# Kernel optimization log

Hardware: AMD Instinct MI355X
Metric: run time of the kernel (lower is better)

The kernel has to match this reference:

```python
import jax, jax.numpy as jnp
import numpy as np
from jax import lax

B, T, C, F_IN = 16, 128, 64, 128
H, FO = 4, 16          # GAT heads, out-features per head (gat_out)
HID = 32               # LSTM hidden (bidirectional -> 64)
NCLS = 3
TOPK, THR, TEMP = 2, 0.3, 1.5


def _layernorm(x, g, b, eps=1e-5):
    m = x.mean(-1, keepdims=True)
    v = ((x - m) ** 2).mean(-1, keepdims=True)
    return (x - m) / jnp.sqrt(v + eps) * g + b


def setup_inputs() -> dict:
    key = jax.random.key(0)
    ks = jax.random.split(key, 16)
    def lin(k, o, i):
        return jax.random.normal(k, (o, i), jnp.float32) / np.sqrt(i)
    return {
        "x": jax.random.uniform(ks[0], (B, T, C, F_IN), jnp.float32),
        "spec_w": jnp.ones((C, F_IN), jnp.float32),
        "gat_W": lin(ks[1], H * FO, F_IN),
        "gat_a": jax.random.normal(ks[2], (H, 2 * FO), jnp.float32),
        "gat_norm_g": jnp.ones((H * FO,), jnp.float32),
        "gat_norm_b": jnp.zeros((H * FO,), jnp.float32),
        "gat_res_W": lin(ks[3], H * FO, F_IN),
        "gat_res_b": jnp.zeros((H * FO,), jnp.float32),
        "lW_ih_f": lin(ks[4], 4 * HID, H * FO),
        "lW_hh_f": lin(ks[5], 4 * HID, HID),
        "lb_ih_f": jnp.zeros((4 * HID,), jnp.float32),
        "lb_hh_f": jnp.zeros((4 * HID,), jnp.float32),
        "lW_ih_b": lin(ks[6], 4 * HID, H * FO),
        "lW_hh_b": lin(ks[7], 4 * HID, HID),
        "lb_ih_b": jnp.zeros((4 * HID,), jnp.float32),
        "lb_hh_b": jnp.zeros((4 * HID,), jnp.float32),
        "ta_W": lin(ks[8], 2 * HID, 2 * HID),
        "ta_b": jnp.zeros((2 * HID,), jnp.float32),
        "ta_v": lin(ks[9], 1, 2 * HID),
        "cp_W": lin(ks[10], 1, 2 * HID),
        "cp_b": jnp.zeros((1,), jnp.float32),
        "norm_g": jnp.ones((2 * HID,), jnp.float32),
        "norm_b": jnp.zeros((2 * HID,), jnp.float32),
        "fc1_W": lin(ks[11], 32, 2 * HID),
        "fc1_b": jnp.zeros((32,), jnp.float32),
        "fc2_W": lin(ks[12], NCLS, 32),
        "fc2_b": jnp.zeros((NCLS,), jnp.float32),
    }


def _lstm(xs, Wih, Whh, bih, bhh):
    # xs: [T, N, in] -> [T, N, HID]; PyTorch gate order i,f,g,o
    N = xs.shape[1]
    def step(carry, xt):
        h, c = carry
        z = xt @ Wih.T + h @ Whh.T + bih + bhh
        i, f, g, o = jnp.split(z, 4, axis=-1)
        c = jax.nn.sigmoid(f) * c + jax.nn.sigmoid(i) * jnp.tanh(g)
        h = jax.nn.sigmoid(o) * jnp.tanh(c)
        return (h, c), h
    init = (jnp.zeros((N, HID), xs.dtype), jnp.zeros((N, HID), xs.dtype))
    return lax.scan(step, init, xs)[1]


def reference(x, spec_w, gat_W, gat_a, gat_norm_g, gat_norm_b, gat_res_W, gat_res_b,
              lW_ih_f, lW_hh_f, lb_ih_f, lb_hh_f, lW_ih_b, lW_hh_b, lb_ih_b, lb_hh_b,
              ta_W, ta_b, ta_v, cp_W, cp_b, norm_g, norm_b,
              fc1_W, fc1_b, fc2_W, fc2_b):
    # --- spectral weighting ---
    x = x * jax.nn.sigmoid(spec_w)                               # [B,T,C,F]
    # --- per-sample correlation graph (vectorized over B,T) ---
    Hn = x / (jnp.linalg.norm(x, axis=-1, keepdims=True) + 1e-8)
    A = jnp.einsum('btcf,btdf->bcd', Hn, Hn) / T                 # mean over T
    A = 0.5 * (A + jnp.swapaxes(A, 1, 2))
    # --- sparsify: per-row top-(k+1), threshold, off-diagonal, symmetrize ---
    _, idx = lax.top_k(A, TOPK + 1)                              # [B,C,k+1]
    topm = jax.nn.one_hot(idx, C).sum(axis=2) > 0                # [B,C,C]
    eye = jnp.eye(C, dtype=bool)
    keep = topm & (A > THR) & ~eye
    keep = keep | jnp.swapaxes(keep, 1, 2)
    A_s = jnp.where(keep, A, 0.0)                                # [B,C,C]
    # --- multi-head GAT, vectorized over all timesteps ---
    Wh = jnp.einsum('btcf,gf->btcg', x, gat_W).reshape(B, T, C, H, FO)
    ei = jnp.einsum('btchf,hf->btch', Wh, gat_a[:, :FO])
    ej = jnp.einsum('btchf,hf->btch', Wh, gat_a[:, FO:])
    e = ei[:, :, :, None, :] + ej[:, :, None, :, :]              # [B,T,C,C,H]
    e = jnp.where(e > 0, e, 0.2 * e)                             # LeakyReLU(0.2)
    mask = (A_s > 0) | eye                                       # [B,C,C]
    e = jnp.where(mask[:, None, :, :, None], e, -1e9)
    An = A_s / (A_s.sum(-1, keepdims=True) + 1e-8)
    e = e + An[:, None, :, :, None]
    alpha = jax.nn.softmax(e / TEMP, axis=3)                     # over j
    Hout = jnp.einsum('btijh,btjhf->btihf', alpha, Wh).reshape(B, T, C, H * FO)
    res = jnp.einsum('btcf,gf->btcg', x, gat_res_W) + gat_res_b
    g = jax.nn.relu(_layernorm(Hout + res, gat_norm_g, gat_norm_b))  # [B,T,C,64]
    # --- BiLSTM over T for each (faithful torch .view on [B,T,C,Fp]) ---
    seq = g.reshape(B * C, T, H * FO)
    xs = jnp.swapaxes(seq, 0, 1)                                 # [T,N,64]
    hf = _lstm(xs, lW_ih_f, lW_hh_f, lb_ih_f, lb_hh_f)
    hb = _lstm(xs[::-1], lW_ih_b, lW_hh_b, lb_ih_b, lb_hh_b)[::-1]
    h = jnp.swapaxes(jnp.concatenate([hf, hb], -1), 0, 1)        # [N,T,64]
    # --- temporal attention ---
    sc = (jnp.tanh(h @ ta_W.T + ta_b) @ ta_v.T)[..., 0]          # [N,T]
    al = jax.nn.softmax(sc / TEMP, axis=1)
    hp = (h * al[..., None]).sum(1)                              # [N,64]
    # --- channel attention pooling ---
    xc = hp.reshape(B, C, 2 * HID)
    w = jax.nn.softmax(xc @ cp_W.T + cp_b, axis=1)               # [B,C,1]
    pooled = (xc * w).sum(1)                                     # [B,64]
    pooled = _layernorm(pooled, norm_g, norm_b)
    hid = jax.nn.relu(pooled @ fc1_W.T + fc1_b)
    return hid @ fc2_W.T + fc2_b                                 # [B,3]
```

## Files before the change

kernel.cpp:

```cpp
#include <hip/hip_runtime.h>
#include <math.h>

#define BB 16
#define TT 128
#define CC 64
#define FF 128

static constexpr float INV_TEMP = 1.0f / 1.5f;

static constexpr size_t OFF_WTT   = 8192;
static constexpr size_t OFF_RTT   = 16384;
static constexpr size_t OFF_TAWT  = 24576;
static constexpr size_t OFF_AN    = 28672;
static constexpr size_t OFF_A     = 94208;
static constexpr size_t OFF_G     = 1208320;
static constexpr size_t OFF_H     = 9596928;
static constexpr size_t OFF_HP    = 17985536;
static constexpr size_t OFF_WIHT  = 18051072;
static constexpr size_t OFF_ZX    = 18067456;
static constexpr size_t OFF_WHS   = OFF_ZX + 16777216;
static constexpr size_t OFF_RS    = OFF_ZX + 25165824;
static constexpr size_t OFF_APART = OFF_WHS;

__global__ __launch_bounds__(256) void k_prep(const float* __restrict__ gat_W,
                                              const float* __restrict__ gat_rW,
                                              const float* __restrict__ ta_W,
                                              const float* __restrict__ Wihf,
                                              const float* __restrict__ Wihb,
                                              float* __restrict__ ws) {
    int i = blockIdx.x * 256 + threadIdx.x;
    if (i < 8192) {
        int k = i >> 6, g = i & 63;
        ws[OFF_WTT + i] = gat_W[g * 128 + k];
    } else if (i < 16384) {
        int j = i - 8192; int k = j >> 6, g = j & 63;
        ws[OFF_RTT + j] = gat_rW[g * 128 + k];
    } else if (i < 20480) {
        int j = i - 16384; int v = j >> 6, u = j & 63;
        ws[OFF_TAWT + j] = ta_W[u * 64 + v];
    } else if (i < 36864) {
        int j = i - 20480;
        int dir = j >> 13, rem = j & 8191, k = rem >> 7, gg = rem & 127;
        const float* W = dir ? Wihb : Wihf;
        ws[OFF_WIHT + j] = W[gg * 64 + k];
    }
}

__device__ __forceinline__ float4 sigmul4(const float4 xv, const float4 wv) {
    float4 o;
    o.x = xv.x / (1.f + __expf(-wv.x));
    o.y = xv.y / (1.f + __expf(-wv.y));
    o.z = xv.z / (1.f + __expf(-wv.z));
    o.w = xv.w / (1.f + __expf(-wv.w));
    return o;
}

__global__ __launch_bounds__(256) void k_corr(const float* __restrict__ x,
                                              const float* __restrict__ spec_w,
                                              float* __restrict__ ws) {
    __shared__ __align__(16) float tile[64 * 132];
    __shared__ float rn[64];
    const int ch = blockIdx.x, b = blockIdx.y, tid = threadIdx.x;
    const int lane = tid & 63, wave = tid >> 6;
    const int c0 = wave * 16 + ((lane >> 4) << 2);
    const int d0 = (lane & 15) << 2;
    const float4* __restrict__ sg4 = (const float4*)spec_w;
    float acc[4][4];
#pragma unroll
    for (int a = 0; a < 4; ++a)
#pragma unroll
        for (int e = 0; e < 4; ++e) acc[a][e] = 0.f;

    for (int t8 = 0; t8 < 2; ++t8) {
        const int t = ch * 2 + t8;
        __syncthreads();
        const float4* __restrict__ xp4 = (const float4*)(x + ((size_t)(b * TT + t)) * CC * FF);
        for (int i4 = tid; i4 < 2048; i4 += 256) {
            const int row = i4 >> 5, col4 = i4 & 31;
            *(float4*)&tile[row * 132 + col4 * 4] = sigmul4(xp4[i4], sg4[i4]);
        }
        __syncthreads();
        {
            const int row = tid >> 2, part = tid & 3;
            const float4* tr = (const float4*)(tile + row * 132 + part * 32);
            float s = 0.f;
#pragma unroll
            for (int q = 0; q < 8; ++q) {
                const float4 v = tr[q];
                s += v.x * v.x + v.y * v.y + v.z * v.z + v.w * v.w;
            }
            s += __shfl_xor(s, 1); s += __shfl_xor(s, 2);
            if (part == 0) rn[row] = 1.f / (sqrtf(s) + 1e-8f);
        }
        __syncthreads();
        float dot[4][4];
#pragma unroll
        for (int a = 0; a < 4; ++a)
#pragma unroll
            for (int e = 0; e < 4; ++e) dot[a][e] = 0.f;
        for (int f4 = 0; f4 < 32; ++f4) {
            float4 xc4[4], xd4[4];
#pragma unroll
            for (int a = 0; a < 4; ++a) xc4[a] = *(const float4*)&tile[(c0 + a) * 132 + f4 * 4];
#pragma unroll
            for (int e = 0; e < 4; ++e) xd4[e] = *(const float4*)&tile[(d0 + e) * 132 + f4 * 4];
#pragma unroll
            for (int a = 0; a < 4; ++a)
#pragma unroll
                for (int e = 0; e < 4; ++e)
                    dot[a][e] += xc4[a].x * xd4[e].x + xc4[a].y * xd4[e].y +
                                 xc4[a].z * xd4[e].z + xc4[a].w * xd4[e].w;
        }
#pragma unroll
        for (int a = 0; a < 4; ++a) {
            const float ra = rn[c0 + a];
#pragma unroll
            for (int e = 0; e < 4; ++e) acc[a][e] += ra * rn[d0 + e] * dot[a][e];
        }
    }
    float* __restrict__ Ap = ws + OFF_APART + ((size_t)(b * 64 + ch)) * 4096;
#pragma unroll
    for (int a = 0; a < 4; ++a)
#pragma unroll
        for (int e = 0; e < 4; ++e) Ap[(c0 + a) * 64 + d0 + e] = acc[a][e];
}

__global__ __launch_bounds__(256) void k_reduceA(float* __restrict__ ws) {
    int i = blockIdx.x * 256 + threadIdx.x;
    int b = i >> 12, e = i & 4095;
    const float* Ap = ws + OFF_APART + (size_t)b * 64 * 4096;
    float s = 0.f;
#pragma unroll 8
    for (int ch = 0; ch < 64; ++ch) s += Ap[ch * 4096 + e];
    ws[OFF_A + i] = s * (1.f / 128.f);
}

__global__ __launch_bounds__(64) void k_sparsify(float* __restrict__ ws) {
    __shared__ float As[64 * 65];
    __shared__ unsigned char kp[64 * 64];
    const int b = blockIdx.x, tid = threadIdx.x;
    const float* Ag = ws + OFF_A + (size_t)b * 4096;
    for (int m = 0; m < 64; ++m) As[m * 65 + tid] = Ag[m * 64 + tid];
    __syncthreads();
    const int c = tid;
    int s0 = -1, s1 = -1, s2 = -1;
    for (int p = 0; p < 3; ++p) {
        float best = -1e30f; int bi = -1;
        for (int d = 0; d < 64; ++d) {
            if (d == s0 || d == s1) continue;
            float v = As[c * 65 + d];
            if (v > best) { best = v; bi = d; }
        }
        if (p == 0) s0 = bi; else if (p == 1) s1 = bi; else s2 = bi;
    }
    for (int d = 0; d < 64; ++d) {
        float v = As[c * 65 + d];
        kp[c * 64 + d] = (unsigned char)(((d == s0) | (d == s1) | (d == s2)) &&
                                         (v > 0.3f) && (d != c));
    }
    __syncthreads();
    float rs = 0.f;
    for (int d = 0; d < 64; ++d) {
        bool k2 = kp[c * 64 + d] || kp[d * 64 + c];
        rs += k2 ? As[c * 65 + d] : 0.f;
    }
    const float inv = 1.f / (rs + 1e-8f);
    float* An = ws + OFF_AN + (size_t)b * 4096;
    for (int d = 0; d < 64; ++d) {
        bool k2 = kp[c * 64 + d] || kp[d * 64 + c];
        An[c * 64 + d] = k2 ? As[c * 65 + d] * inv : 0.f;
    }
}

__global__ __launch_bounds__(256) void k_wh(const float* __restrict__ x,
                                            const float* __restrict__ spec_w,
                                            const float* __restrict__ wt,
                                            const float* __restrict__ rt,
                                            float* __restrict__ whs,
                                            float* __restrict__ rs,
                                            const float* __restrict__ res_b) {
    __shared__ __align__(16) float tile[64 * 132];
    const int bt = blockIdx.x, tid = threadIdx.x;
    const float4* __restrict__ xp4 = (const float4*)(x + (size_t)bt * 8192);
    const float4* __restrict__ sg4 = (const float4*)spec_w;
    for (int i4 = tid; i4 < 2048; i4 += 256) {
        const int row = i4 >> 5, col4 = i4 & 31;
        *(float4*)&tile[row * 132 + col4 * 4] = sigmul4(xp4[i4], sg4[i4]);
    }
    __syncthreads();
    const int tx = tid & 31, ty = tid >> 5;
    const int mat = tx >> 4, cx = tx & 15;
    const int r0 = ty * 8, c0 = cx * 4;
    const float* __restrict__ wbase = mat ? rt : wt;
    float acc[8][4];
#pragma unroll
    for (int i = 0; i < 8; ++i)
#pragma unroll
        for (int j = 0; j < 4; ++j) acc[i][j] = 0.f;
    for (int k4 = 0; k4 < 32; ++k4) {
        float xs[8][4];
#pragma unroll
        for (int i = 0; i < 8; ++i) {
            const float4 v = *(const float4*)&tile[(r0 + i) * 132 + k4 * 4];
            xs[i][0] = v.x; xs[i][1] = v.y; xs[i][2] = v.z; xs[i][3] = v.w;
        }
#pragma unroll
        for (int kk = 0; kk < 4; ++kk) {
            const float4 wv = *(const float4*)(wbase + (k4 * 4 + kk) * 64 + c0);
#pragma unroll
            for (int i = 0; i < 8; ++i) {
                acc[i][0] += xs[i][kk] * wv.x;
                acc[i][1] += xs[i][kk] * wv.y;
                acc[i][2] += xs[i][kk] * wv.z;
                acc[i][3] += xs[i][kk] * wv.w;
            }
        }
    }
    if (mat == 0) {
        float* __restrict__ op = whs + (size_t)bt * 4096;
#pragma unroll
        for (int i = 0; i < 8; ++i) {
            float4 o; o.x = acc[i][0]; o.y = acc[i][1]; o.z = acc[i][2]; o.w = acc[i][3];
            *(float4*)(op + (r0 + i) * 64 + c0) = o;
        }
    } else {
        const float4 rb = *(const float4*)(res_b + c0);
        float* __restrict__ op = rs + (size_t)bt * 4096;
#pragma unroll
        for (int i = 0; i < 8; ++i) {
            float4 o; o.x = acc[i][0] + rb.x; o.y = acc[i][1] + rb.y;
            o.z = acc[i][2] + rb.z; o.w = acc[i][3] + rb.w;
            *(float4*)(op + (r0 + i) * 64 + c0) = o;
        }
    }
}

__global__ __launch_bounds__(256) void k_att(const float* __restrict__ ws,
                                             const float* __restrict__ whs,
                                             const float* __restrict__ rs,
                                             float* __restrict__ g,
                                             const float* __restrict__ gat_a,
                                             const float* __restrict__ ln_g,
                                             const float* __restrict__ ln_b) {
    __shared__ __align__(16) float sWh[64 * 68];
    __shared__ float sAn[64 * 65];
    __shared__ float sEjT[256];
    __shared__ float sStat[64 * 8];
    const int t = blockIdx.x, b = blockIdx.y, tid = threadIdx.x;
    const size_t bt = (size_t)(b * TT + t);
    const float4* __restrict__ wh4 = (const float4*)(whs + bt * 4096);
    for (int i4 = tid; i4 < 1024; i4 += 256) {
        const int row = i4 >> 4, c4 = i4 & 15;
        *(float4*)&sWh[row * 68 + c4 * 4] = wh4[i4];
    }
    const float* __restrict__ ang = ws + OFF_AN + (size_t)b * 4096;
    for (int i = tid; i < 4096; i += 256) sAn[(i >> 6) * 65 + (i & 63)] = ang[i];
    __syncthreads();

    const int ia = tid & 63, ha = tid >> 6;
    float eiv = 0.f, ejv = 0.f;
    {
        const float* __restrict__ whrow = sWh + ia * 68 + ha * 16;
        const float* __restrict__ aip = gat_a + ha * 32;
#pragma unroll
        for (int q = 0; q < 16; ++q) {
            const float w = whrow[q];
            eiv += w * aip[q];
            ejv += w * aip[16 + q];
        }
    }
    sEjT[ha * 64 + ia] = ejv;
    __syncthreads();

    float ao[16];
#pragma unroll
    for (int f = 0; f < 16; ++f) ao[f] = 0.f;
    float sum = 0.f;
    const float* __restrict__ anrow = sAn + ia * 65;
    const float* __restrict__ ejrow = sEjT + ha * 64;
#pragma unroll 4
    for (int j = 0; j < 64; ++j) {
        const float s = eiv + ejrow[j];
        const float l = s > 0.f ? s : 0.2f * s;
        const float anv = anrow[j];
        const float z = (anv != 0.f || j == ia) ? (l + anv) : -1e9f;
        const float p = __expf(z * INV_TEMP);
        sum += p;
        const float* __restrict__ wj = sWh + j * 68 + ha * 16;
        const float4 w0 = *(const float4*)(wj);
        const float4 w1 = *(const float4*)(wj + 4);
        const float4 w2 = *(const float4*)(wj + 8);
        const float4 w3 = *(const float4*)(wj + 12);
        ao[0]  += p * w0.x; ao[1]  += p * w0.y; ao[2]  += p * w0.z; ao[3]  += p * w0.w;
        ao[4]  += p * w1.x; ao[5]  += p * w1.y; ao[6]  += p * w1.z; ao[7]  += p * w1.w;
        ao[8]  += p * w2.x; ao[9]  += p * w2.y; ao[10] += p * w2.z; ao[11] += p * w2.w;
        ao[12] += p * w3.x; ao[13] += p * w3.y; ao[14] += p * w3.z; ao[15] += p * w3.w;
    }
    const float inv = 1.f / sum;
    float val[16];
    float s1 = 0.f, s2 = 0.f;
    const float* __restrict__ rsp = rs + bt * 4096 + ia * 64 + ha * 16;
#pragma unroll
    for (int q = 0; q < 4; ++q) {
        const float4 rv = *(const float4*)(rsp + q * 4);
        val[q * 4 + 0] = ao[q * 4 + 0] * inv + rv.x;
        val[q * 4 + 1] = ao[q * 4 + 1] * inv + rv.y;
        val[q * 4 + 2] = ao[q * 4 + 2] * inv + rv.z;
        val[q * 4 + 3] = ao[q * 4 + 3] * inv + rv.w;
    }
#pragma unroll
    for (int f = 0; f < 16; ++f) { s1 += val[f]; s2 += val[f] * val[f]; }
    sStat[ia * 8 + ha] = s1;
    sStat[ia * 8 + 4 + ha] = s2;
    __syncthreads();
    const float tsum = sStat[ia * 8 + 0] + sStat[ia * 8 + 1] + sStat[ia * 8 + 2] + sStat[ia * 8 + 3];
    const float tsq  = sStat[ia * 8 + 4] + sStat[ia * 8 + 5] + sStat[ia * 8 + 6] + sStat[ia * 8 + 7];
    const float mean = tsum * (1.f / 64.f);
    const float var = tsq * (1.f / 64.f) - mean * mean;
    const float rstd = rsqrtf(var + 1e-5f);
    float* __restrict__ gout = g + bt * 4096 + ia * 64 + ha * 16;
#pragma unroll
    for (int q = 0; q < 4; ++q) {
        const float4 gm = *(const float4*)(ln_g + ha * 16 + q * 4);
        const float4 bt4 = *(const float4*)(ln_b + ha * 16 + q * 4);
        float4 o;
        o.x = fmaxf((val[q * 4 + 0] - mean) * rstd * gm.x + bt4.x, 0.f);
        o.y = fmaxf((val[q * 4 + 1] - mean) * rstd * gm.y + bt4.y, 0.f);
        o.z = fmaxf((val[q * 4 + 2] - mean) * rstd * gm.z + bt4.z, 0.f);
        o.w = fmaxf((val[q * 4 + 3] - mean) * rstd * gm.w + bt4.w, 0.f);
        *(float4*)(gout + q * 4) = o;
    }
}

__global__ __launch_bounds__(256) void k_zx(const float* __restrict__ gbuf,
                                            const float* __restrict__ ws,
                                            float* __restrict__ zx,
                                            const float* __restrict__ bihf, const float* __restrict__ bhhf,
                                            const float* __restrict__ bihb, const float* __restrict__ bhhb) {
    __shared__ __align__(16) float gS[128 * 68];
    const int mt2 = blockIdx.x, dir = blockIdx.y, tid = threadIdx.x;
    const float4* __restrict__ gsrc4 = (const float4*)(gbuf + (size_t)mt2 * 8192);
    for (int i4 = tid; i4 < 2048; i4 += 256) {
        const int row = i4 >> 4, c4 = i4 & 15;
        *(float4*)&gS[row * 68 + c4 * 4] = gsrc4[i4];
    }
    __syncthreads();
    const int ty = tid >> 4, cxx = tid & 15;
    const int c0 = cxx * 8;
    const float* __restrict__ wT = ws + OFF_WIHT + (size_t)dir * 8192;
    float acc[8][8];
#pragma unroll
    for (int i = 0; i < 8; ++i)
#pragma unroll
        for (int j = 0; j < 8; ++j) acc[i][j] = 0.f;
    for (int k4 = 0; k4 < 16; ++k4) {
        float xs[8][4];
#pragma unroll
        for (int i = 0; i < 8; ++i) {
            const float4 v = *(const float4*)&gS[(ty + 16 * i) * 68 + k4 * 4];
            xs[i][0] = v.x; xs[i][1] = v.y; xs[i][2] = v.z; xs[i][3] = v.w;
        }
#pragma unroll
        for (int kk = 0; kk < 4; ++kk) {
            const float4 w0 = *(const float4*)(wT + (k4 * 4 + kk) * 128 + c0);
            const float4 w1 = *(const float4*)(wT + (k4 * 4 + kk) * 128 + c0 + 4);
#pragma unroll
            for (int i = 0; i < 8; ++i) {
                const float xv = xs[i][kk];
                acc[i][0] += xv * w0.x; acc[i][1] += xv * w0.y;
                acc[i][2] += xv * w0.z; acc[i][3] += xv * w0.w;
                acc[i][4] += xv * w1.x; acc[i][5] += xv * w1.y;
                acc[i][6] += xv * w1.z; acc[i][7] += xv * w1.w;
            }
        }
    }
    const float* bi = dir ? bihb : bihf;
    const float* bh = dir ? bhhb : bhhf;
    float bsum[8];
    {
        const float4 b0 = *(const float4*)(bi + c0), b1 = *(const float4*)(bi + c0 + 4);
        const float4 h0 = *(const float4*)(bh + c0), h1 = *(const float4*)(bh + c0 + 4);
        bsum[0] = b0.x + h0.x; bsum[1] = b0.y + h0.y; bsum[2] = b0.z + h0.z; bsum[3] = b0.w + h0.w;
        bsum[4] = b1.x + h1.x; bsum[5] = b1.y + h1.y; bsum[6] = b1.z + h1.z; bsum[7] = b1.w + h1.w;
    }
    float* __restrict__ zrow = zx + (size_t)dir * 16777216 + (size_t)mt2 * 16384;
#pragma unroll
    for (int i = 0; i < 8; ++i) {
        const int r = ty + 16 * i;
        float4 o0, o1;
        o0.x = acc[i][0] + bsum[0]; o0.y = acc[i][1] + bsum[1];
        o0.z = acc[i][2] + bsum[2]; o0.w = acc[i][3] + bsum[3];
        o1.x = acc[i][4] + bsum[4]; o1.y = acc[i][5] + bsum[5];
        o1.z = acc[i][6] + bsum[6]; o1.w = acc[i][7] + bsum[7];
        *(float4*)&zrow[r * 128 + c0] = o0;
        *(float4*)&zrow[r * 128 + c0 + 4] = o1;
    }
}

__device__ __forceinline__ float rl(float v, int l) {
    return __int_as_float(__builtin_amdgcn_readlane(__float_as_int(v), l));
}

__global__ __launch_bounds__(64, 1) void k_lstm6(const float* __restrict__ zx,
                                                 float* __restrict__ hbuf,
                                                 const float* __restrict__ Whhf,
                                                 const float* __restrict__ Whhb) {
    __shared__ __align__(16) float swb[128 * 36];
    const int n = blockIdx.x, dir = blockIdx.y, r = threadIdx.x;
    const bool lo = (r < 32);
    const float* __restrict__ Whh = dir ? Whhb : Whhf;
    const float4* W4 = (const float4*)Whh;
    {
        float4* sw = (float4*)swb;
#pragma unroll
        for (int m = 0; m < 16; ++m) {
            const int idx = r + 64 * m;
            const int j = idx >> 3, q = idx & 7;
            sw[j * 9 + q] = W4[idx];
        }
    }
    __syncthreads();
    const float4* sw4 = (const float4*)swb;
    int baseA = r * 9;
    int baseB = (r + 64) * 9;
    const float* __restrict__ zxp = zx + (size_t)dir * 16777216 + (size_t)n * 16384;
    float* __restrict__ hout = hbuf + (size_t)n * 8192 + dir * 32 + r;
    float hv = 0.f, cv = 0.f;

#define SADDR(S_) (zxp + (size_t)(dir ? 127 - (S_) : (S_)) * 128)
#define DOTQL(Q) {                                                          \
        const float4 u = sw4[baseA + Q];                                    \
        const float4 v = sw4[baseB + Q];                                    \
        const float h0 = rl(hv, 4 * Q + 0), h1 = rl(hv, 4 * Q + 1);         \
        const float h2 = rl(hv, 4 * Q + 2), h3 = rl(hv, 4 * Q + 3);         \
        a0 += h0 * u.x; b0 += h0 * v.x;                                     \
        a1 += h1 * u.y; b1 += h1 * v.y;                                     \
        a0 += h2 * u.z; b0 += h2 * v.z;                                     \
        a1 += h3 * u.w; b1 += h3 * v.w;                                     \
    }
#define STEP(S_, ZA, ZB) {                                                  \
        asm volatile("" : "+v"(baseA), "+v"(baseB));                        \
        float a0 = (ZA), a1 = 0.f, b0 = (ZB), b1 = 0.f;                     \
        DOTQL(0) DOTQL(1) DOTQL(2) DOTQL(3)                                 \
        DOTQL(4) DOTQL(5) DOTQL(6) DOTQL(7)                                 \
        const float zi = a0 + a1, zg = b0 + b1;                             \
        const float eA = __expf(-zi);                                       \
        const float sA = 1.f / (1.f + eA);                                  \
        const float eB = __expf(lo ? -2.f * zg : -zg);                      \
        const float vB = lo ? (2.f / (1.f + eB) - 1.f) : (1.f / (1.f + eB));\
        const float fv = __shfl_xor(sA, 32);                                \
        const float ox = __shfl_xor(vB, 32);                                \
        cv = fv * cv + sA * vB;                                             \
        const float eC = __expf(-2.f * cv);                                 \
        const float tc = 2.f / (1.f + eC) - 1.f;                            \
        hv = ox * tc;                                                       \
        const int s__ = dir ? 127 - (S_) : (S_);                            \
        if (lo) hout[s__ * 64] = hv;                                        \
    }

    const float* p0 = SADDR(0);
    const float* p1 = SADDR(1);
    float zA0 = p0[r], zB0 = p0[r + 64];
    float zA1 = p1[r], zB1 = p1[r + 64];
    for (int s2 = 0; s2 < 64; ++s2) {
        int sp = 2 * s2 + 2; if (sp > 126) sp = 126;
        const float* pn0 = SADDR(sp);
        const float* pn1 = SADDR(sp + 1);
        const float nA0 = pn0[r], nB0 = pn0[r + 64];
        const float nA1 = pn1[r], nB1 = pn1[r + 64];
        STEP(2 * s2, zA0, zB0);
        STEP(2 * s2 + 1, zA1, zB1);
        zA0 = nA0; zB0 = nB0; zA1 = nA1; zB1 = nB1;
    }
#undef STEP
#undef DOTQL
#undef SADDR
}

__global__ __launch_bounds__(256) void k_ta(float* __restrict__ ws,
                                            const float* __restrict__ tab,
                                            const float* __restrict__ tav) {
    __shared__ __align__(16) float hL[128 * 68];
    __shared__ float scL[128];
    __shared__ float sRed[4];
    __shared__ float sPart[256];
    const int n = blockIdx.x, tid = threadIdx.x, lane = tid & 63, wave = tid >> 6;
    const float4* __restrict__ hsrc4 = (const float4*)(ws + OFF_H + (size_t)n * 8192);
    for (int i4 = tid; i4 < 2048; i4 += 256) {
        const int row = i4 >> 4, c4 = i4 & 15;
        *(float4*)&hL[row * 68 + c4 * 4] = hsrc4[i4];
    }
    __syncthreads();
    const int ty8 = lane >> 3, ux = lane & 7;
    const int t0 = wave * 32 + ty8, u0 = ux * 8;
    const float* __restrict__ twt = ws + OFF_TAWT;
    float tb[8], tv[8];
    *(float4*)&tb[0] = *(const float4*)(tab + u0);
    *(float4*)&tb[4] = *(const float4*)(tab + u0 + 4);
    *(float4*)&tv[0] = *(const float4*)(tav + u0);
    *(float4*)&tv[4] = *(const float4*)(tav + u0 + 4);
    float a[4][8];
#pragma unroll
    for (int i = 0; i < 4; ++i)
#pragma unroll
        for (int j = 0; j < 8; ++j) a[i][j] = 0.f;
    for (int v4 = 0; v4 < 16; ++v4) {
        float xs[4][4];
#pragma unroll
        for (int i = 0; i < 4; ++i) {
            const float4 v = *(const float4*)&hL[(t0 + 8 * i) * 68 + v4 * 4];
            xs[i][0] = v.x; xs[i][1] = v.y; xs[i][2] = v.z; xs[i][3] = v.w;
        }
#pragma unroll
        for (int kk = 0; kk < 4; ++kk) {
            const float4 w0 = *(const float4*)(twt + (v4 * 4 + kk) * 64 + u0);
            const float4 w1 = *(const float4*)(twt + (v4 * 4 + kk) * 64 + u0 + 4);
#pragma unroll
            for (int i = 0; i < 4; ++i) {
                const float xv = xs[i][kk];
                a[i][0] += xv * w0.x; a[i][1] += xv * w0.y;
                a[i][2] += xv * w0.z; a[i][3] += xv * w0.w;
                a[i][4] += xv * w1.x; a[i][5] += xv * w1.y;
                a[i][6] += xv * w1.z; a[i][7] += xv * w1.w;
            }
        }
    }
#pragma unroll
    for (int i = 0; i < 4; ++i) {
        float s = 0.f;
#pragma unroll
        for (int u = 0; u < 8; ++u) s += tanhf(a[i][u] + tb[u]) * tv[u];
        s += __shfl_xor(s, 1); s += __shfl_xor(s, 2); s += __shfl_xor(s, 4);
        if (ux == 0) scL[t0 + 8 * i] = s;
    }
    __syncthreads();
    const float v = (tid < 128) ? scL[tid] : -1e30f;
    float mw = v;
    mw = fmaxf(mw, __shfl_xor(mw, 1)); mw = fmaxf(mw, __shfl_xor(mw, 2));
    mw = fmaxf(mw, __shfl_xor(mw, 4)); mw = fmaxf(mw, __shfl_xor(mw, 8));
    mw = fmaxf(mw, __shfl_xor(mw, 16)); mw = fmaxf(mw, __shfl_xor(mw, 32));
    if (lane == 0) sRed[wave] = mw;
    __syncthreads();
    const float m = fmaxf(fmaxf(sRed[0], sRed[1]), fmaxf(sRed[2], sRed[3]));
    const float p = (tid < 128) ? __expf((v - m) * INV_TEMP) : 0.f;
    float sw = p;
    sw += __shfl_xor(sw, 1); sw += __shfl_xor(sw, 2); sw += __shfl_xor(sw, 4);
    sw += __shfl_xor(sw, 8); sw += __shfl_xor(sw, 16); sw += __shfl_xor(sw, 32);
    __syncthreads();
    if (lane == 0) sRed[wave] = sw;
    __syncthreads();
    const float stot = sRed[0] + sRed[1] + sRed[2] + sRed[3];
    if (tid < 128) scL[tid] = p / stot;
    __syncthreads();
    float part = 0.f;
    for (int tt = 0; tt < 32; ++tt) {
        const int t = wave * 32 + tt;
        part += scL[t] * hL[t * 68 + lane];
    }
    sPart[wave * 64 + lane] = part;
    __syncthreads();
    if (tid < 64)
        ws[OFF_HP + (size_t)n * 64 + tid] =
            sPart[tid] + sPart[64 + tid] + sPart[128 + tid] + sPart[192 + tid];
}

__global__ __launch_bounds__(64) void k_final(const float* __restrict__ ws,
                                              const float* __restrict__ cpW, const float* __restrict__ cpb,
                                              const float* __restrict__ ng, const float* __restrict__ nb,
                                              const float* __restrict__ f1W, const float* __restrict__ f1b,
                                              const float* __restrict__ f2W, const float* __restrict__ f2b,
                                              float* __restrict__ out) {
    __shared__ float xc[64 * 65];
    __shared__ float wL[64];
    __shared__ float plL[64];
    __shared__ float h1L[32];
    const int b = blockIdx.x, tid = threadIdx.x;
    const float* hp = ws + OFF_HP + (size_t)b * 4096;
    for (int m = 0; m < 64; ++m) xc[m * 65 + tid] = hp[m * 64 + tid];
    __syncthreads();
    float s = cpb[0];
    for (int j = 0; j < 64; ++j) s += xc[tid * 65 + j] * cpW[j];
    float mm = s;
    for (int o = 1; o < 64; o <<= 1) mm = fmaxf(mm, __shfl_xor(mm, o));
    const float p = __expf(s - mm);
    float sum = p;
    for (int o = 1; o < 64; o <<= 1) sum += __shfl_xor(sum, o);
    wL[tid] = p / sum;
    __syncthreads();
    float pool = 0.f;
    for (int c = 0; c < 64; ++c) pool += xc[c * 65 + tid] * wL[c];
    float ms = pool;
    for (int o = 1; o < 64; o <<= 1) ms += __shfl_xor(ms, o);
    const float mean = ms * (1.f / 64.f);
    const float d = pool - mean;
    float vv = d * d;
    for (int o = 1; o < 64; o <<= 1) vv += __shfl_xor(vv, o);
    const float pl = d * rsqrtf(vv * (1.f / 64.f) + 1e-5f) * ng[tid] + nb[tid];
    plL[tid] = pl;
    __syncthreads();
    if (tid < 32) {
        float h1 = f1b[tid];
        for (int j = 0; j < 64; ++j) h1 += plL[j] * f1W[tid * 64 + j];
        h1L[tid] = fmaxf(h1, 0.f);
    }
    __syncthreads();
    if (tid < 3) {
        float o = f2b[tid];
        for (int uu = 0; uu < 32; ++uu) o += h1L[uu] * f2W[tid * 32 + uu];
        out[b * 3 + tid] = o;
    }
}

extern "C" void kernel_launch(void* const* d_in, const int* in_sizes, int n_in,
                              void* d_out, int out_size, void* d_ws, size_t ws_size,
                              hipStream_t stream) {
    (void)in_sizes; (void)n_in; (void)out_size; (void)ws_size;
    const float* x      = (const float*)d_in[0];
    const float* spec_w = (const float*)d_in[1];
    const float* gat_W  = (const float*)d_in[2];
    const float* gat_a  = (const float*)d_in[3];
    const float* gat_ng = (const float*)d_in[4];
    const float* gat_nb = (const float*)d_in[5];
    const float* gat_rW = (const float*)d_in[6];
    const float* gat_rb = (const float*)d_in[7];
    const float* Wihf   = (const float*)d_in[8];
    const float* Whhf   = (const float*)d_in[9];
    const float* bihf   = (const float*)d_in[10];
    const float* bhhf   = (const float*)d_in[11];
    const float* Wihb   = (const float*)d_in[12];
    const float* Whhb   = (const float*)d_in[13];
    const float* bihb   = (const float*)d_in[14];
    const float* bhhb   = (const float*)d_in[15];
    const float* ta_W   = (const float*)d_in[16];
    const float* ta_b   = (const float*)d_in[17];
    const float* ta_v   = (const float*)d_in[18];
    const float* cp_W   = (const float*)d_in[19];
    const float* cp_b   = (const float*)d_in[20];
    const float* norm_g = (const float*)d_in[21];
    const float* norm_b = (const float*)d_in[22];
    const float* fc1_W  = (const float*)d_in[23];
    const float* fc1_b  = (const float*)d_in[24];
    const float* fc2_W  = (const float*)d_in[25];
    const float* fc2_b  = (const float*)d_in[26];
    float* ws  = (float*)d_ws;
    float* out = (float*)d_out;

    hipLaunchKernelGGL(k_prep, dim3(144), dim3(256), 0, stream, gat_W, gat_rW, ta_W, Wihf, Wihb, ws);
    hipLaunchKernelGGL(k_corr, dim3(64, 16), dim3(256), 0, stream, x, spec_w, ws);
    hipLaunchKernelGGL(k_reduceA, dim3(256), dim3(256), 0, stream, ws);
    hipLaunchKernelGGL(k_sparsify, dim3(16), dim3(64), 0, stream, ws);
    hipLaunchKernelGGL(k_wh, dim3(2048), dim3(256), 0, stream,
                       x, spec_w, ws + OFF_WTT, ws + OFF_RTT,
                       ws + OFF_WHS, ws + OFF_RS, gat_rb);
    hipLaunchKernelGGL(k_att, dim3(128, 16), dim3(256), 0, stream,
                       ws, ws + OFF_WHS, ws + OFF_RS, ws + OFF_G,
                       gat_a, gat_ng, gat_nb);
    hipLaunchKernelGGL(k_zx, dim3(1024, 2), dim3(256), 0, stream,
                       ws + OFF_G, ws, ws + OFF_ZX, bihf, bhhf, bihb, bhhb);
    hipLaunchKernelGGL(k_lstm6, dim3(1024, 2), dim3(64), 0, stream,
                       ws + OFF_ZX, ws + OFF_H, Whhf, Whhb);
    hipLaunchKernelGGL(k_ta, dim3(1024), dim3(256), 0, stream, ws, ta_b, ta_v);
    hipLaunchKernelGGL(k_final, dim3(16), dim3(64), 0, stream, ws, cp_W, cp_b,
                       norm_g, norm_b, fc1_W, fc1_b, fc2_W, fc2_b, out);
}
```

Baseline: 390.5 us.

## Process two sequences per LSTM wave to share weights and add ILP

```diff
diff --git a/kernel.cpp b/kernel.cpp
--- a/kernel.cpp
+++ b/kernel.cpp
@@ -401,12 +401,12 @@
     return __int_as_float(__builtin_amdgcn_readlane(__float_as_int(v), l));
 }
 
-__global__ __launch_bounds__(64, 1) void k_lstm6(const float* __restrict__ zx,
+__global__ __launch_bounds__(64, 1) void k_lstm7(const float* __restrict__ zx,
                                                  float* __restrict__ hbuf,
                                                  const float* __restrict__ Whhf,
                                                  const float* __restrict__ Whhb) {
     __shared__ __align__(16) float swb[128 * 36];
-    const int n = blockIdx.x, dir = blockIdx.y, r = threadIdx.x;
+    const int n0 = blockIdx.x * 2, dir = blockIdx.y, r = threadIdx.x;
     const bool lo = (r < 32);
     const float* __restrict__ Whh = dir ? Whhb : Whhf;
     const float4* W4 = (const float4*)Whh;
@@ -423,58 +423,80 @@
     const float4* sw4 = (const float4*)swb;
     int baseA = r * 9;
     int baseB = (r + 64) * 9;
-    const float* __restrict__ zxp = zx + (size_t)dir * 16777216 + (size_t)n * 16384;
-    float* __restrict__ hout = hbuf + (size_t)n * 8192 + dir * 32 + r;
-    float hv = 0.f, cv = 0.f;
-
-#define SADDR(S_) (zxp + (size_t)(dir ? 127 - (S_) : (S_)) * 128)
-#define DOTQL(Q) {                                                          \
+    const float* __restrict__ zxp0 = zx + (size_t)dir * 16777216 + (size_t)n0 * 16384;
+    const float* __restrict__ zxp1 = zxp0 + 16384;
+    float* __restrict__ hout0 = hbuf + (size_t)n0 * 8192 + dir * 32 + r;
+    float* __restrict__ hout1 = hout0 + 8192;
+    float hv0 = 0.f, cv0 = 0.f, hv1 = 0.f, cv1 = 0.f;
+
+#define SADDR0(S_) (zxp0 + (size_t)(dir ? 127 - (S_) : (S_)) * 128)
+#define SADDR1(S_) (zxp1 + (size_t)(dir ? 127 - (S_) : (S_)) * 128)
+#define DOTQ2(Q) {                                                          \
         const float4 u = sw4[baseA + Q];                                    \
         const float4 v = sw4[baseB + Q];                                    \
-        const float h0 = rl(hv, 4 * Q + 0), h1 = rl(hv, 4 * Q + 1);         \
-        const float h2 = rl(hv, 4 * Q + 2), h3 = rl(hv, 4 * Q + 3);         \
-        a0 += h0 * u.x; b0 += h0 * v.x;                                     \
-        a1 += h1 * u.y; b1 += h1 * v.y;                                     \
-        a0 += h2 * u.z; b0 += h2 * v.z;                                     \
-        a1 += h3 * u.w; b1 += h3 * v.w;                                     \
-    }
-#define STEP(S_, ZA, ZB) {                                                  \
-        asm volatile("" : "+v"(baseA), "+v"(baseB));                        \
-        float a0 = (ZA), a1 = 0.f, b0 = (ZB), b1 = 0.f;                     \
-        DOTQL(0) DOTQL(1) DOTQL(2) DOTQL(3)                                 \
-        DOTQL(4) DOTQL(5) DOTQL(6) DOTQL(7)                                 \
-        const float zi = a0 + a1, zg = b0 + b1;                             \
-        const float eA = __expf(-zi);                                       \
+        {   const float h0 = rl(hv0, 4 * Q + 0), h1 = rl(hv0, 4 * Q + 1);   \
+            const float h2 = rl(hv0, 4 * Q + 2), h3 = rl(hv0, 4 * Q + 3);   \
+            a00 += h0 * u.x; b00 += h0 * v.x;                               \
+            a10 += h1 * u.y; b10 += h1 * v.y;                               \
+            a00 += h2 * u.z; b00 += h2 * v.z;                               \
+            a10 += h3 * u.w; b10 += h3 * v.w; }                             \
+        {   const float h0 = rl(hv1, 4 * Q + 0), h1 = rl(hv1, 4 * Q + 1);   \
+            const float h2 = rl(hv1, 4 * Q + 2), h3 = rl(hv1, 4 * Q + 3);   \
+            a01 += h0 * u.x; b01 += h0 * v.x;                               \
+            a11 += h1 * u.y; b11 += h1 * v.y;                               \
+            a01 += h2 * u.z; b01 += h2 * v.z;                               \
+            a11 += h3 * u.w; b11 += h3 * v.w; }                             \
+    }
+#define ACT(ZI, ZG, HV, CV, HOUT) {                                         \
+        const float eA = __expf(-(ZI));                                     \
         const float sA = 1.f / (1.f + eA);                                  \
-        const float eB = __expf(lo ? -2.f * zg : -zg);                      \
+        const float eB = __expf(lo ? -2.f * (ZG) : -(ZG));                  \
         const float vB = lo ? (2.f / (1.f + eB) - 1.f) : (1.f / (1.f + eB));\
         const float fv = __shfl_xor(sA, 32);                                \
         const float ox = __shfl_xor(vB, 32);                                \
-        cv = fv * cv + sA * vB;                                             \
-        const float eC = __expf(-2.f * cv);                                 \
+        CV = fv * CV + sA * vB;                                             \
+        const float eC = __expf(-2.f * CV);                                 \
         const float tc = 2.f / (1.f + eC) - 1.f;                            \
-        hv = ox * tc;                                                       \
+        HV = ox * tc;                                                       \
+        if (lo) HOUT[s__ * 64] = HV;                                        \
+    }
+#define STEP2(S_, ZA0, ZB0, ZA1, ZB1) {                                     \
+        asm volatile("" : "+v"(baseA), "+v"(baseB));                        \
+        float a00 = (ZA0), a10 = 0.f, b00 = (ZB0), b10 = 0.f;               \
+        float a01 = (ZA1), a11 = 0.f, b01 = (ZB1), b11 = 0.f;               \
+        DOTQ2(0) DOTQ2(1) DOTQ2(2) DOTQ2(3)                                 \
+        DOTQ2(4) DOTQ2(5) DOTQ2(6) DOTQ2(7)                                 \
         const int s__ = dir ? 127 - (S_) : (S_);                            \
-        if (lo) hout[s__ * 64] = hv;                                        \
-    }
-
-    const float* p0 = SADDR(0);
-    const float* p1 = SADDR(1);
-    float zA0 = p0[r], zB0 = p0[r + 64];
-    float zA1 = p1[r], zB1 = p1[r + 64];
+        ACT(a00 + a10, b00 + b10, hv0, cv0, hout0)                          \
+        ACT(a01 + a11, b01 + b11, hv1, cv1, hout1)                          \
+    }
+
+    const float* q00 = SADDR0(0);
+    const float* q01 = SADDR0(1);
+    const float* q10 = SADDR1(0);
+    const float* q11 = SADDR1(1);
+    float e0A = q00[r], e0B = q00[r + 64], o0A = q01[r], o0B = q01[r + 64];
+    float e1A = q10[r], e1B = q10[r + 64], o1A = q11[r], o1B = q11[r + 64];
     for (int s2 = 0; s2 < 64; ++s2) {
         int sp = 2 * s2 + 2; if (sp > 126) sp = 126;
-        const float* pn0 = SADDR(sp);
-        const float* pn1 = SADDR(sp + 1);
-        const float nA0 = pn0[r], nB0 = pn0[r + 64];
-        const float nA1 = pn1[r], nB1 = pn1[r + 64];
-        STEP(2 * s2, zA0, zB0);
-        STEP(2 * s2 + 1, zA1, zB1);
-        zA0 = nA0; zB0 = nB0; zA1 = nA1; zB1 = nB1;
-    }
-#undef STEP
-#undef DOTQL
-#undef SADDR
+        const float* pn00 = SADDR0(sp);
+        const float* pn01 = SADDR0(sp + 1);
+        const float* pn10 = SADDR1(sp);
+        const float* pn11 = SADDR1(sp + 1);
+        const float nA00 = pn00[r], nB00 = pn00[r + 64];
+        const float nA01 = pn01[r], nB01 = pn01[r + 64];
+        const float nA10 = pn10[r], nB10 = pn10[r + 64];
+        const float nA11 = pn11[r], nB11 = pn11[r + 64];
+        STEP2(2 * s2,     e0A, e0B, e1A, e1B);
+        STEP2(2 * s2 + 1, o0A, o0B, o1A, o1B);
+        e0A = nA00; e0B = nB00; o0A = nA01; o0B = nB01;
+        e1A = nA10; e1B = nB10; o1A = nA11; o1B = nB11;
+    }
+#undef STEP2
+#undef ACT
+#undef DOTQ2
+#undef SADDR0
+#undef SADDR1
 }
 
 __global__ __launch_bounds__(256) void k_ta(float* __restrict__ ws,
@@ -657,7 +679,7 @@
                        gat_a, gat_ng, gat_nb);
     hipLaunchKernelGGL(k_zx, dim3(1024, 2), dim3(256), 0, stream,
                        ws + OFF_G, ws, ws + OFF_ZX, bihf, bhhf, bihb, bhhb);
-    hipLaunchKernelGGL(k_lstm6, dim3(1024, 2), dim3(64), 0, stream,
+    hipLaunchKernelGGL(k_lstm7, dim3(512, 2), dim3(64), 0, stream,
                        ws + OFF_ZX, ws + OFF_H, Whhf, Whhb);
     hipLaunchKernelGGL(k_ta, dim3(1024), dim3(256), 0, stream, ws, ta_b, ta_v);
     hipLaunchKernelGGL(k_final, dim3(16), dim3(64), 0, stream, ws, cp_W, cp_b,
```

Result: slower. 464.5 us (+18.9%).
